# Optimization experiments

Hardware: AMD Instinct MI355X
Metric: run time of the kernel (lower is better)

Reference implementation:

```python
import jax, jax.numpy as jnp
import numpy as np

B, N, D, H, G = 4, 2048, 384, 8, 512
K = 8            # knn neighbors (hardcoded in get_graph_feature)
HID = 4 * D      # mlp_ratio = 4
FIN = 3 + G      # fuse_mlp in_features


def _ln(x, g, b, eps=1e-5):
    m = x.mean(-1, keepdims=True)
    v = ((x - m) ** 2).mean(-1, keepdims=True)
    return (x - m) * jax.lax.rsqrt(v + eps) * g + b


def _self_attn(x, qkv_w, pw, pb):
    b, n, c = x.shape
    hd = c // H
    qkv = (x @ qkv_w).reshape(b, n, 3, H, hd).transpose(2, 0, 3, 1, 4)
    q, k, v = qkv[0], qkv[1], qkv[2]                      # [b,h,n,hd]
    a = jax.nn.softmax(jnp.einsum('bhnd,bhmd->bhnm', q, k) * hd ** -0.5, -1)
    o = jnp.einsum('bhnm,bhmd->bhnd', a, v).transpose(0, 2, 1, 3).reshape(b, n, c)
    return o @ pw + pb


def _cross_attn(q, v, qw, kw, vw, pw, pb):
    b, n, c = q.shape
    nk = v.shape[1]
    hd = c // H
    qh = (q @ qw).reshape(b, n, H, hd).transpose(0, 2, 1, 3)
    kh = (v @ kw).reshape(b, nk, H, hd).transpose(0, 2, 1, 3)
    vh = (v @ vw).reshape(b, nk, H, hd).transpose(0, 2, 1, 3)
    a = jax.nn.softmax(jnp.einsum('bhnd,bhmd->bhnm', qh, kh) * hd ** -0.5, -1)
    o = jnp.einsum('bhnm,bhmd->bhnd', a, vh).transpose(0, 2, 1, 3).reshape(b, n, c)
    return o @ pw + pb


def _graph_feature(x, knn_index, x_q=None):
    b, n, c = x.shape
    nq = x_q.shape[1] if x_q is not None else n
    feat = x.reshape(b * n, c)[knn_index.reshape(-1)].reshape(b, K, nq, c)
    xq = (x_q if x_q is not None else x)[:, None, :, :]   # [b,1,nq,c]
    return jnp.concatenate([feat - xq, jnp.broadcast_to(xq, feat.shape)], -1)


def setup_inputs():
    key = jax.random.key(0)
    ks = iter(jax.random.split(key, 32))
    nrm = lambda shape: jax.random.normal(next(ks), shape, jnp.float32) * 0.02
    f32 = jnp.float32
    inp = {
        'q': jax.random.normal(next(ks), (B, D, N), f32),
        'in_pos': jax.random.normal(next(ks), (B, 3, N), f32),
        'guide_coding': jax.random.normal(next(ks), (B, G), f32),
        'norm1_g': jnp.ones((D,), f32), 'norm1_b': jnp.zeros((D,), f32),
        'qkv_w': nrm((D, 3 * D)),
        'sa_proj_w': nrm((D, D)), 'sa_proj_b': jnp.zeros((D,), f32),
        'normq_g': jnp.ones((D,), f32), 'normq_b': jnp.zeros((D,), f32),
        'fuse1_w': nrm((FIN, FIN)), 'fuse1_b': jnp.zeros((FIN,), f32),
        'fuse2_w': nrm((FIN, D)), 'fuse2_b': jnp.zeros((D,), f32),
        'normv_g': jnp.ones((D,), f32), 'normv_b': jnp.zeros((D,), f32),
        'ca_q_w': nrm((D, D)), 'ca_k_w': nrm((D, D)), 'ca_v_w': nrm((D, D)),
        'ca_proj_w': nrm((D, D)), 'ca_proj_b': jnp.zeros((D,), f32),
        'norm2_g': jnp.ones((D,), f32), 'norm2_b': jnp.zeros((D,), f32),
        'mlp1_w': nrm((D, HID)), 'mlp1_b': jnp.zeros((HID,), f32),
        'mlp2_w': nrm((HID, D)), 'mlp2_b': jnp.zeros((D,), f32),
        'knn_w': nrm((2 * D, D)), 'knn_b': jnp.zeros((D,), f32),
        'merge_w': nrm((2 * D, D)), 'merge_b': jnp.zeros((D,), f32),
        'knnx_w': nrm((2 * D, D)), 'knnx_b': jnp.zeros((D,), f32),
        'mergex_w': nrm((2 * D, D)), 'mergex_b': jnp.zeros((D,), f32),
        'self_knn_index': jax.random.randint(next(ks), (B, K, N), 0, B * N),
        'cross_knn_index': jax.random.randint(next(ks), (B, K, N), 0, B * N),
    }
    return inp


def reference(q, in_pos, guide_coding, norm1_g, norm1_b, qkv_w, sa_proj_w, sa_proj_b,
              normq_g, normq_b, fuse1_w, fuse1_b, fuse2_w, fuse2_b, normv_g, normv_b,
              ca_q_w, ca_k_w, ca_v_w, ca_proj_w, ca_proj_b, norm2_g, norm2_b,
              mlp1_w, mlp1_b, mlp2_w, mlp2_b, knn_w, knn_b, merge_w, merge_b,
              knnx_w, knnx_b, mergex_w, mergex_b, self_knn_index, cross_knn_index):
    npoints = in_pos.shape[2]
    q = q.transpose(0, 2, 1)                              # [B,N,D]
    norm_q = _ln(q, norm1_g, norm1_b)
    q_1 = _self_attn(norm_q, qkv_w, sa_proj_w, sa_proj_b)
    # build v from positions + broadcast guide coding
    gc = jnp.broadcast_to(guide_coding[:, :, None], (q.shape[0], G, npoints))
    v = jnp.concatenate([in_pos, gc], axis=1).transpose(0, 2, 1)  # [B,N,3+G]
    v = jax.nn.gelu(v @ fuse1_w + fuse1_b, approximate=False) @ fuse2_w + fuse2_b
    # self knn branch
    knn_f = _graph_feature(norm_q, self_knn_index)        # [B,K,N,2D]
    knn_f = jax.nn.leaky_relu(knn_f @ knn_w + knn_b, 0.2).max(axis=1)
    q_1 = jnp.concatenate([q_1, knn_f], -1) @ merge_w + merge_b
    q = q + q_1
    norm_q = _ln(q, normq_g, normq_b)
    norm_v = _ln(v, normv_g, normv_b)
    q_2 = _cross_attn(norm_q, norm_v, ca_q_w, ca_k_w, ca_v_w, ca_proj_w, ca_proj_b)
    # cross knn branch
    knn_f = _graph_feature(norm_v, cross_knn_index, norm_q)
    knn_f = jax.nn.leaky_relu(knn_f @ knnx_w + knnx_b, 0.2).max(axis=1)
    q_2 = jnp.concatenate([q_2, knn_f], -1) @ mergex_w + mergex_b
    q = q + q_2
    h = _ln(q, norm2_g, norm2_b)
    q = q + (jax.nn.gelu(h @ mlp1_w + mlp1_b, approximate=False) @ mlp2_w + mlp2_b)
    return q.transpose(0, 2, 1)                           # [B,D,N]
```

## Files before the change

### kernel.cpp

```cpp
#include <hip/hip_runtime.h>
#include <cstdint>
#include <cstddef>

#define B_ 4
#define N_ 2048
#define D_ 384
#define H_ 8
#define HD_ 48
#define G_ 512
#define K_ 8
#define HID_ 1536
#define FIN_ 515
#define FINP_ 576
#define M_ (B_*N_)
#define QSCALE 0.20823512f

typedef unsigned short u16;
typedef __attribute__((ext_vector_type(8))) short bf16x8;
typedef __attribute__((ext_vector_type(4))) float f32x4;

#define GLOAD16(gp, lp) __builtin_amdgcn_global_load_lds( \
    (const __attribute__((address_space(1))) void*)(gp), \
    (__attribute__((address_space(3))) void*)(lp), 16, 0, 0)

__device__ __forceinline__ u16 f2bf(float x){
  unsigned u = __builtin_bit_cast(unsigned, x);
  unsigned r = (u + 0x7fffu + ((u >> 16) & 1u)) >> 16;
  return (u16)r;
}
__device__ __forceinline__ float bf2f(u16 v){
  unsigned u = ((unsigned)v) << 16;
  return __builtin_bit_cast(float, u);
}
__device__ __forceinline__ float exp2_hw(float x){
  float r;
  asm("v_exp_f32 %0, %1" : "=v"(r) : "v"(x));
  return r;
}
__device__ __forceinline__ float gelu_f(float x){
  return 0.5f*x*(1.f + erff(x*0.70710678118654752f));
}

__global__ __launch_bounds__(256) void transpose_k(const float* __restrict__ in,
    float* __restrict__ out, int R, int C){
  __shared__ float tile[32][33];
  int b = blockIdx.z;
  int c0 = blockIdx.x<<5, r0 = blockIdx.y<<5;
  const float* ip = in + (size_t)b*R*C;
  float* op = out + (size_t)b*R*C;
  int tx = threadIdx.x, ty = threadIdx.y;
  #pragma unroll
  for (int i = ty; i < 32; i += 8)
    tile[i][tx] = ip[(size_t)(r0+i)*C + c0 + tx];
  __syncthreads();
  #pragma unroll
  for (int i = ty; i < 32; i += 8)
    op[(size_t)(c0+i)*R + r0 + tx] = tile[tx][i];
}

struct WJob { const float* src; u16* dst; int Kd, Nd, Kp, diff, Np, nbx, blk0; };
struct WJobs { WJob j[16]; };

__global__ __launch_bounds__(256) void wtconv_all(WJobs J){
  int b = blockIdx.x, ji = 0;
  #pragma unroll
  for (int i=1;i<16;i++) if (b >= J.j[i].blk0) ji = i;
  WJob jb = J.j[ji];
  int local = b - jb.blk0;
  int bx = local % jb.nbx, by = local / jb.nbx;
  __shared__ float tile[32][33];
  int k0 = bx<<5, n0 = by<<5;
  int tx = threadIdx.x, ty = threadIdx.y;
  #pragma unroll
  for (int i = ty; i < 32; i += 8){
    int k = k0+i, n = n0+tx;
    float v = 0.f;
    if (k < jb.Kd && n < jb.Nd){
      v = jb.src[(size_t)k*jb.Nd + n];
      if (jb.diff) v = jb.src[(size_t)(k+jb.diff)*jb.Nd + n] - v;
    }
    tile[i][tx] = v;
  }
  __syncthreads();
  #pragma unroll
  for (int i = ty; i < 32; i += 8){
    int n = n0+i, k = k0+tx;
    if (n < jb.Np && k < jb.Kp) jb.dst[(size_t)n*jb.Kp + k] = f2bf(tile[tx][i]);
  }
}

struct WP { const float *pw, *mwt, *pb, *mb2; u16* W; float* Bo; };
__global__ __launch_bounds__(256) void wprod_k(WP a, WP b){
  WP w = blockIdx.y ? b : a;
  int idx = blockIdx.x*256 + threadIdx.x;
  if (idx >= 385*384) return;
  int n = idx % 384, kk = idx / 384;
  float acc = 0.f;
  if (kk < 384){
    for (int j=0;j<384;j++) acc += w.pw[(size_t)kk*384+j] * w.mwt[(size_t)j*384+n];
    w.W[(size_t)n*768 + kk] = f2bf(acc);
  } else {
    for (int j=0;j<384;j++) acc += w.pb[j] * w.mwt[(size_t)j*384+n];
    w.Bo[n] = acc + w.mb2[n];
  }
}

__global__ __launch_bounds__(256) void biasfill_k(const float* __restrict__ knnb,
    const float* __restrict__ knnxb, float* __restrict__ bws){
  int i = blockIdx.x*256 + threadIdx.x;
  if (i < 2688){
    float v = 0.f;
    if (i >= 1536 && i < 1920) v = knnb[i-1536];
    else if (i >= 2304) v = knnxb[i-2304];
    bws[i] = v;
  }
}

__device__ __forceinline__ void ln_body(const float* xr, const float* g,
    const float* bta, u16* yr, float* sbuf, int t){
  float v0 = xr[t], v1 = xr[t+128], v2 = xr[t+256];
  float s = v0+v1+v2;
  #pragma unroll
  for (int off=32; off>0; off>>=1) s += __shfl_down(s, off, 64);
  int lane = t & 63, w = t >> 6;
  if (lane==0) sbuf[w] = s;
  __syncthreads();
  float mean = (sbuf[0]+sbuf[1]) * (1.f/(float)D_);
  float d0 = v0-mean, d1 = v1-mean, d2 = v2-mean;
  float s2 = d0*d0 + d1*d1 + d2*d2;
  #pragma unroll
  for (int off=32; off>0; off>>=1) s2 += __shfl_down(s2, off, 64);
  __syncthreads();
  if (lane==0) sbuf[w] = s2;
  __syncthreads();
  float inv = rsqrtf((sbuf[0]+sbuf[1])*(1.f/(float)D_) + 1e-5f);
  yr[t]     = f2bf(d0*inv*g[t]     + bta[t]);
  yr[t+128] = f2bf(d1*inv*g[t+128] + bta[t+128]);
  yr[t+256] = f2bf(d2*inv*g[t+256] + bta[t+256]);
}

__global__ __launch_bounds__(128) void ln_bf(const float* __restrict__ x,
    const float* __restrict__ g, const float* __restrict__ bta, u16* __restrict__ y){
  __shared__ float sbuf[2];
  int row = blockIdx.x;
  ln_body(x + (size_t)row*D_, g, bta, y + (size_t)row*D_, sbuf, threadIdx.x);
}

__global__ __launch_bounds__(128) void ln2_bf(const float* __restrict__ x0,
    const float* __restrict__ g0, const float* __restrict__ b0, u16* __restrict__ y0,
    const float* __restrict__ x1, const float* __restrict__ g1,
    const float* __restrict__ b1, u16* __restrict__ y1){
  __shared__ float sbuf[2];
  int row = blockIdx.x;
  if (row < M_)
    ln_body(x0 + (size_t)row*D_, g0, b0, y0 + (size_t)row*D_, sbuf, threadIdx.x);
  else {
    row -= M_;
    ln_body(x1 + (size_t)row*D_, g1, b1, y1 + (size_t)row*D_, sbuf, threadIdx.x);
  }
}

template<int ACT, int OUTBF, int ACCUM, int HASBIAS, int SCALEQ>
__global__ __launch_bounds__(512) void gemm8(const u16* __restrict__ A, int lda,
    const u16* __restrict__ Wt, int ldw, const float* __restrict__ bias,
    float* __restrict__ Cf, u16* __restrict__ Cb, int ldc, int Kd, int Nd, int Npad){
  __shared__ char Lmem[33280];
  u16* As = (u16*)Lmem;
  u16* Bs = As + 128*64;
  float* cred = (float*)Lmem;
  const int t = threadIdx.x;
  const int wv = t>>6, l = t&63;
  const int kg = wv>>2, wq = wv&3;
  const int wm = wq&1, wn = wq>>1;
  const int lr = l&15, ls = l>>4;
  const int bm = blockIdx.y<<7, bn = blockIdx.x<<6;
  f32x4 z4 = {0.f,0.f,0.f,0.f};
  f32x4 acc[4][2];
  #pragma unroll
  for (int mi=0;mi<4;mi++){ acc[mi][0]=z4; acc[mi][1]=z4; }
  int ago[2];
  #pragma unroll
  for (int i=0;i<2;i++){
    int g = t + (i<<9);
    int row = g>>3, slot = g&7;
    ago[i] = row*lda + ((slot ^ (row&7))<<3);
  }
  int bgo;
  {
    int row = t>>3, slot = t&7;
    bgo = row*ldw + ((slot ^ (row&7))<<3);
  }
  const u16* Abase = A + (size_t)bm*lda;
  const u16* Bbase = Wt + (size_t)bn*ldw;
  for (int k0=0; k0<Kd; k0+=64){
    #pragma unroll
    for (int i=0;i<2;i++)
      GLOAD16(Abase + k0 + ago[i], (char*)As + ((t + (i<<9))<<4));
    GLOAD16(Bbase + k0 + bgo, (char*)Bs + (t<<4));
    __syncthreads();
    bf16x8 af[4], bfr[2];
    #pragma unroll
    for (int mi=0;mi<4;mi++){
      int row = wm*64 + mi*16 + lr;
      int ss = (kg*4 + ls) ^ (row&7);
      af[mi] = *reinterpret_cast<bf16x8*>((char*)As + row*128 + ss*16);
    }
    #pragma unroll
    for (int ni=0;ni<2;ni++){
      int row = wn*32 + ni*16 + lr;
      int ss = (kg*4 + ls) ^ (row&7);
      bfr[ni] = *reinterpret_cast<bf16x8*>((char*)Bs + row*128 + ss*16);
    }
    #pragma unroll
    for (int mi=0;mi<4;mi++)
      #pragma unroll
      for (int ni=0;ni<2;ni++)
        acc[mi][ni] = __builtin_amdgcn_mfma_f32_16x16x32_bf16(af[mi], bfr[ni], acc[mi][ni], 0,0,0);
    __syncthreads();
  }
  if (kg == 1){
    #pragma unroll
    for (int mi=0;mi<4;mi++)
      #pragma unroll
      for (int ni=0;ni<2;ni++)
        #pragma unroll
        for (int r=0;r<4;r++){
          int row = wm*64 + mi*16 + ls*4 + r;
          int col = wn*32 + ni*16 + lr;
          cred[row*65 + col] = acc[mi][ni][r];
        }
  }
  __syncthreads();
  if (kg == 0){
    #pragma unroll
    for (int mi=0;mi<4;mi++){
      #pragma unroll
      for (int ni=0;ni<2;ni++){
        #pragma unroll
        for (int r=0;r<4;r++){
          int rl = wm*64 + mi*16 + ls*4 + r;
          int cl = wn*32 + ni*16 + lr;
          int row = bm + rl, col = bn + cl;
          float v = acc[mi][ni][r] + cred[rl*65 + cl];
          if (col < Nd){
            if (SCALEQ && col < 384) v *= QSCALE;
            if (HASBIAS) v += bias[col];
            if (ACT) v = gelu_f(v);
            if (OUTBF) Cb[(size_t)row*ldc + col] = f2bf(v);
            else if (ACCUM) Cf[(size_t)row*ldc + col] += v;
            else Cf[(size_t)row*ldc + col] = v;
          } else if (OUTBF && col < Npad){
            Cb[(size_t)row*ldc + col] = 0;
          }
        }
      }
    }
  }
}

__global__ __launch_bounds__(256) void vt_k(const u16* __restrict__ X, int ld,
                                            u16* __restrict__ Vt){
  __shared__ u16 tl[64][72];
  int bh = blockIdx.y, b = bh>>3, h = bh&7;
  int n0 = blockIdx.x<<6;
  #pragma unroll
  for (int i=0;i<2;i++){
    int g = threadIdx.x + (i<<8);
    if (g < 384){
      int r = g/6, c = (g - r*6)*8;
      *reinterpret_cast<float4*>(&tl[r][c]) =
        *reinterpret_cast<const float4*>(X + (size_t)(b*N_ + n0 + r)*ld + h*HD_ + c);
    }
  }
  __syncthreads();
  #pragma unroll
  for (int i=0;i<2;i++){
    int g = threadIdx.x + (i<<8);
    if (g < 384){
      int d = g % 48, sb = g / 48;
      int hf = (n0>>6)&1;
      int kt0 = n0 & ~127;
      size_t rowb = ((size_t)(bh*HD_+d))*N_ + kt0;
      int kA = hf*64 + sb*8;
      ushort4 va, vb;
      va.x = tl[sb*8+0][d]; va.y = tl[sb*8+1][d];
      va.z = tl[sb*8+2][d]; va.w = tl[sb*8+3][d];
      vb.x = tl[sb*8+4][d]; vb.y = tl[sb*8+5][d];
      vb.z = tl[sb*8+6][d]; vb.w = tl[sb*8+7][d];
      int uA = ((kA>>5)<<2) | ((kA>>2)&3);
      int pA = (((uA ^ (d&15)))<<3) + (((kA>>4)&1)<<2);
      int kB = kA + 4;
      int uB = ((kB>>5)<<2) | ((kB>>2)&3);
      int pB = (((uB ^ (d&15)))<<3) + (((kB>>4)&1)<<2);
      *reinterpret_cast<ushort4*>(Vt + rowb + pA) = va;
      *reinterpret_cast<ushort4*>(Vt + rowb + pB) = vb;
    }
  }
}

__global__ __launch_bounds__(256) void attn_mfma(const u16* __restrict__ Qp, int ldq,
    const u16* __restrict__ Kp, int ldk, const u16* __restrict__ Vt,
    u16* __restrict__ O, int ldo){
  __shared__ __align__(16) char KVls[2][28672];
  const int t = threadIdx.x, wv = t>>6, l = t&63;
  const int lr = l&15, ls = l>>4;
  const int bh = blockIdx.y, bb = bh>>3, h = bh&7;
  const int q0 = blockIdx.x<<6;
  bf16x8 zf = {0,0,0,0,0,0,0,0};
  f32x4 z4 = {0.f,0.f,0.f,0.f};
  const size_t rowQ = ((size_t)(bb*N_ + q0 + wv*16 + lr))*ldq + h*HD_;
  bf16x8 qa0 = *reinterpret_cast<const bf16x8*>(Qp + rowQ + 8*ls);
  bf16x8 qa1 = (ls < 2) ? *reinterpret_cast<const bf16x8*>(Qp + rowQ + 32 + 8*ls) : zf;
  f32x4 oacc[3] = {z4, z4, z4};
  float mrun = -1.0e30f, lrun = 0.f;

  const u16* Kbase = Kp + (size_t)(bb*N_)*ldk + h*HD_;
  const u16* Vbase = Vt + (size_t)bh*HD_*N_;
  int kgo[4];
  #pragma unroll
  for (int i=0;i<4;i++){
    int g = t + (i<<8);
    int key = g>>3, s = g&7;
    kgo[i] = key*ldk + ((s ^ (key&7))<<3);
  }
  int vgo[3];
  #pragma unroll
  for (int i=0;i<3;i++){
    int g = t + (i<<8);
    int d = g>>4, s = g&15;
    vgo[i] = d*N_ + (s<<3);
  }

  auto stage = [&](int kt, char* buf){
    const u16* kp = Kbase + (size_t)kt*128*ldk;
    #pragma unroll
    for (int i=0;i<4;i++)
      GLOAD16(kp + kgo[i], buf + ((t + (i<<8))<<4));
    const u16* vp = Vbase + kt*128;
    #pragma unroll
    for (int i=0;i<3;i++)
      GLOAD16(vp + vgo[i], buf + 16384 + ((t + (i<<8))<<4));
  };

  stage(0, KVls[0]);
  for (int kt = 0; kt < N_/128; kt++){
    char* cbuf = KVls[kt&1];
    if (kt+1 < N_/128){
      stage(kt+1, KVls[(kt+1)&1]);
      asm volatile("s_waitcnt vmcnt(7)" ::: "memory");
    } else {
      asm volatile("s_waitcnt vmcnt(0)" ::: "memory");
    }
    __builtin_amdgcn_sched_barrier(0);
    __builtin_amdgcn_s_barrier();
    __builtin_amdgcn_sched_barrier(0);
    f32x4 S[8];
    __builtin_amdgcn_s_setprio(1);
    #pragma unroll
    for (int sub=0; sub<8; sub++){
      int krow = sub*16 + lr;
      bf16x8 kb0 = *reinterpret_cast<bf16x8*>(cbuf + krow*128 + ((ls ^ (krow&7))<<4));
      bf16x8 kb1 = *reinterpret_cast<bf16x8*>(cbuf + krow*128 + (((4+ls) ^ (krow&7))<<4));
      f32x4 s = __builtin_amdgcn_mfma_f32_16x16x32_bf16(kb0, qa0, z4, 0,0,0);
      S[sub] = __builtin_amdgcn_mfma_f32_16x16x32_bf16(kb1, qa1, s, 0,0,0);
    }
    __builtin_amdgcn_s_setprio(0);
    float tm = fmaxf(fmaxf(fmaxf(S[0][0],S[0][1]), fmaxf(S[0][2],S[0][3])),
                     fmaxf(fmaxf(S[1][0],S[1][1]), fmaxf(S[1][2],S[1][3])));
    #pragma unroll
    for (int sub=2;sub<8;sub++)
      tm = fmaxf(tm, fmaxf(fmaxf(S[sub][0],S[sub][1]), fmaxf(S[sub][2],S[sub][3])));
    if (__all(tm - mrun <= 10.f)){
      float ps = 0.f;
      #pragma unroll
      for (int sub=0;sub<8;sub++)
        #pragma unroll
        for (int r=0;r<4;r++){
          float p = exp2_hw(S[sub][r]-mrun);
          S[sub][r] = p; ps += p;
        }
      lrun += ps;
    } else {
      float mx = fmaxf(tm, __shfl_xor(tm, 16, 64));
      mx = fmaxf(mx, __shfl_xor(mx, 32, 64));
      float mnew = fmaxf(mrun, mx);
      float al = exp2_hw(mrun - mnew);
      mrun = mnew;
      float ps = 0.f;
      #pragma unroll
      for (int sub=0;sub<8;sub++)
        #pragma unroll
        for (int r=0;r<4;r++){
          float p = exp2_hw(S[sub][r]-mnew);
          S[sub][r] = p; ps += p;
        }
      lrun = lrun*al + ps;
      #pragma unroll
      for (int r=0;r<4;r++){
        float alq = __shfl(al, ls*4 + r, 64);
        oacc[0][r] *= alq; oacc[1][r] *= alq; oacc[2][r] *= alq;
      }
    }
    union PU { unsigned u[4]; bf16x8 v; };
    PU pa[4];
    #pragma unroll
    for (int kb=0;kb<4;kb++){
      asm("v_cvt_pk_bf16_f32 %0, %1, %2" : "=v"(pa[kb].u[0]) : "v"(S[2*kb][0]),   "v"(S[2*kb][1]));
      asm("v_cvt_pk_bf16_f32 %0, %1, %2" : "=v"(pa[kb].u[1]) : "v"(S[2*kb][2]),   "v"(S[2*kb][3]));
      asm("v_cvt_pk_bf16_f32 %0, %1, %2" : "=v"(pa[kb].u[2]) : "v"(S[2*kb+1][0]), "v"(S[2*kb+1][1]));
      asm("v_cvt_pk_bf16_f32 %0, %1, %2" : "=v"(pa[kb].u[3]) : "v"(S[2*kb+1][2]), "v"(S[2*kb+1][3]));
    }
    __builtin_amdgcn_s_setprio(1);
    #pragma unroll
    for (int ni=0;ni<3;ni++){
      int d = ni*16 + lr;
      #pragma unroll
      for (int kb=0;kb<4;kb++){
        bf16x8 vb = *reinterpret_cast<bf16x8*>(cbuf + 16384 + d*256 + ((((kb*4+ls) ^ (d&15)))<<4));
        oacc[ni] = __builtin_amdgcn_mfma_f32_16x16x32_bf16(pa[kb].v, vb, oacc[ni], 0,0,0);
      }
    }
    __builtin_amdgcn_s_setprio(0);
    __builtin_amdgcn_sched_barrier(0);
    __builtin_amdgcn_s_barrier();
    __builtin_amdgcn_sched_barrier(0);
  }
  float sden = lrun;
  sden += __shfl_xor(sden, 16, 64);
  sden += __shfl_xor(sden, 32, 64);
  #pragma unroll
  for (int r=0;r<4;r++){
    float dq = __shfl(sden, ls*4 + r, 64);
    float inv = 1.f / dq;
    size_t orow = (size_t)(bb*N_ + q0 + wv*16 + ls*4 + r);
    #pragma unroll
    for (int ni=0;ni<3;ni++)
      O[orow*ldo + h*HD_ + ni*16 + lr] = f2bf(oacc[ni][r] * inv);
  }
}

__global__ __launch_bounds__(384) void gather_max_bf(const u16* __restrict__ P, int ldp,
    const u16* __restrict__ Q2, int ldq2, const int* __restrict__ idx,
    u16* __restrict__ out, int ldo){
  int m = blockIdx.x;
  int d = threadIdx.x;
  int b = m >> 11, n = m & (N_-1);
  float q2 = bf2f(Q2[(size_t)m*ldq2 + d]);
  float mx = -3.0e38f;
  #pragma unroll
  for (int k=0;k<K_;k++){
    int j = idx[((b<<3) + k)*N_ + n];
    float val = bf2f(P[(size_t)j*ldp + d]) + q2;
    val = (val >= 0.f) ? val : 0.2f*val;
    mx = fmaxf(mx, val);
  }
  out[(size_t)m*ldo + d] = f2bf(mx);
}

__global__ __launch_bounds__(256) void build_v(const float* __restrict__ pos,
    const float* __restrict__ gc, u16* __restrict__ v){
  int m = blockIdx.x;
  int b = m >> 11, n = m & (N_-1);
  for (int c = threadIdx.x; c < FINP_; c += 256){
    float val = 0.f;
    if (c < 3) val = pos[(b*3 + c)*N_ + n];
    else if (c < FIN_) val = gc[(b<<9) + (c-3)];
    v[(size_t)m*FINP_ + c] = f2bf(val);
  }
}

extern "C" void kernel_launch(void* const* d_in, const int* in_sizes, int n_in,
                              void* d_out, int out_size, void* d_ws, size_t ws_size,
                              hipStream_t stream){
  const float* q_in   = (const float*)d_in[0];
  const float* in_pos = (const float*)d_in[1];
  const float* guide  = (const float*)d_in[2];
  const float* n1g = (const float*)d_in[3];
  const float* n1b = (const float*)d_in[4];
  const float* qkv_w = (const float*)d_in[5];
  const float* sa_pw = (const float*)d_in[6];
  const float* sa_pb = (const float*)d_in[7];
  const float* nqg = (const float*)d_in[8];
  const float* nqb = (const float*)d_in[9];
  const float* f1w = (const float*)d_in[10];
  const float* f1b = (const float*)d_in[11];
  const float* f2w = (const float*)d_in[12];
  const float* f2b = (const float*)d_in[13];
  const float* nvg = (const float*)d_in[14];
  const float* nvb = (const float*)d_in[15];
  const float* caqw = (const float*)d_in[16];
  const float* cakw = (const float*)d_in[17];
  const float* cavw = (const float*)d_in[18];
  const float* capw = (const float*)d_in[19];
  const float* capb = (const float*)d_in[20];
  const float* n2g = (const float*)d_in[21];
  const float* n2b = (const float*)d_in[22];
  const float* m1w = (const float*)d_in[23];
  const float* m1b = (const float*)d_in[24];
  const float* m2w = (const float*)d_in[25];
  const float* m2b = (const float*)d_in[26];
  const float* knnw = (const float*)d_in[27];
  const float* knnb = (const float*)d_in[28];
  const float* mw = (const float*)d_in[29];
  const float* mb = (const float*)d_in[30];
  const float* knnxw = (const float*)d_in[31];
  const float* knnxb = (const float*)d_in[32];
  const float* mxw = (const float*)d_in[33];
  const float* mxb = (const float*)d_in[34];
  const int* sidx = (const int*)d_in[35];
  const int* cidx = (const int*)d_in[36];
  float* out = (float*)d_out;

  const size_t MD = (size_t)M_*D_;
  float* q_cur = (float*)d_ws;
  float* vbuf  = q_cur + MD;
  u16* R     = (u16*)(vbuf + MD);
  u16* nq_bf = R + (size_t)M_*1920;
  u16* nv_bf = nq_bf + MD;
  u16* cc    = nv_bf + MD;
  u16* vin   = cc + (size_t)M_*768;
  u16* e2    = vin + (size_t)M_*FINP_;
  u16* Vt    = e2 + (size_t)M_*FINP_;
  u16* wb    = Vt + (size_t)32*HD_*N_;
  u16* W1    = wb;  wb += (size_t)1920*384;
  u16* Wq    = wb;  wb += (size_t)768*384;
  u16* Wv    = wb;  wb += (size_t)1152*384;
  u16* Wfold = wb;  wb += (size_t)384*768;
  u16* Wfoldx= wb;  wb += (size_t)384*768;
  u16* f1T   = wb;  wb += (size_t)FINP_*FINP_;
  u16* f2T   = wb;  wb += (size_t)384*FINP_;
  u16* m1T   = wb;  wb += (size_t)1536*384;
  u16* m2T   = wb;  wb += (size_t)384*1536;
  if (((uintptr_t)wb & 3) != 0) wb++;
  float* bias_ws = (float*)wb;
  const size_t needed = (char*)(bias_ws + 3456) - (char*)d_ws;
  if (ws_size < needed) return;

  u16* X1 = R;
  u16* Xq = R;
  u16* Xv = R + (size_t)M_*768;
  u16* hid = R;

  dim3 tb32(32,8);
  transpose_k<<<dim3(N_/32, D_/32, B_), tb32, 0, stream>>>(q_in, q_cur, D_, N_);
  WJobs J;
  auto setj = [&](int i, const float* src, u16* dst, int Kd, int Nd, int Kp, int diff, int Np){
    J.j[i].src = src; J.j[i].dst = dst; J.j[i].Kd = Kd; J.j[i].Nd = Nd;
    J.j[i].Kp = Kp; J.j[i].diff = diff; J.j[i].Np = Np;
    J.j[i].nbx = (Kp+31)/32; J.j[i].blk0 = 0;
  };
  setj(0,  qkv_w, W1,                    384, 1152, 384, 0,   1152);
  setj(1,  knnw,  W1 + (size_t)1152*384, 384, 384, 384, 0,    384);
  setj(2,  knnw,  W1 + (size_t)1536*384, 384, 384, 384, 384,  384);
  setj(3,  caqw,  Wq,                    384, 384, 384, 0,    384);
  setj(4,  knnxw, Wq + (size_t)384*384,  384, 384, 384, 384,  384);
  setj(5,  cakw,  Wv,                    384, 384, 384, 0,    384);
  setj(6,  cavw,  Wv + (size_t)384*384,  384, 384, 384, 0,    384);
  setj(7,  knnxw, Wv + (size_t)768*384,  384, 384, 384, 0,    384);
  setj(8,  mw  + (size_t)384*384, Wfold  + 384, 384, 384, 768, 0, 384);
  setj(9,  mxw + (size_t)384*384, Wfoldx + 384, 384, 384, 768, 0, 384);
  setj(10, f1w,   f1T, FIN_, FIN_, FINP_, 0, FINP_);
  setj(11, f2w,   f2T, FIN_, 384, FINP_, 0,  384);
  setj(12, m1w,   m1T, 384, 1536, 384, 0,    1536);
  setj(13, m2w,   m2T, 1536, 384, 1536, 0,   384);
  int tot = 0;
  for (int i=0;i<14;i++){ J.j[i].blk0 = tot; tot += J.j[i].nbx * ((J.j[i].Np+31)/32); }
  J.j[14] = J.j[13]; J.j[14].blk0 = 0x7fffffff; J.j[14].nbx = 1;
  J.j[15] = J.j[14];
  wtconv_all<<<tot, tb32, 0, stream>>>(J);
  WP wpa = { sa_pw, mw,  sa_pb, mb,  Wfold,  bias_ws + 2688 };
  WP wpb = { capw,  mxw, capb,  mxb, Wfoldx, bias_ws + 3072 };
  wprod_k<<<dim3(578, 2), 256, 0, stream>>>(wpa, wpb);
  biasfill_k<<<11, 256, 0, stream>>>(knnb, knnxb, bias_ws);
  ln_bf<<<M_, 128, 0, stream>>>(q_cur, n1g, n1b, nq_bf);
  gemm8<0,1,0,1,1><<<dim3(30, 64), 512, 0, stream>>>(nq_bf, 384, W1, 384, bias_ws, nullptr, X1, 1920, 384, 1920, 1920);
  vt_k<<<dim3(32, 32), 256, 0, stream>>>(X1 + 768, 1920, Vt);
  attn_mfma<<<dim3(32, 32), 256, 0, stream>>>(X1, 1920, X1 + 384, 1920, Vt, cc, 768);
  gather_max_bf<<<M_, 384, 0, stream>>>(X1 + 1152, 1920, X1 + 1536, 1920, sidx, cc + 384, 768);
  gemm8<0,0,1,1,0><<<dim3(6, 64), 512, 0, stream>>>(cc, 768, Wfold, 768, bias_ws + 2688, q_cur, nullptr, 384, 768, 384, 384);
  build_v<<<M_, 256, 0, stream>>>(in_pos, guide, vin);
  gemm8<1,1,0,1,0><<<dim3(9, 64), 512, 0, stream>>>(vin, FINP_, f1T, FINP_, f1b, nullptr, e2, FINP_, FINP_, FIN_, FINP_);
  gemm8<0,0,0,1,0><<<dim3(6, 64), 512, 0, stream>>>(e2, FINP_, f2T, FINP_, f2b, vbuf, nullptr, 384, FINP_, 384, 384);
  ln2_bf<<<2*M_, 128, 0, stream>>>(q_cur, nqg, nqb, nq_bf, vbuf, nvg, nvb, nv_bf);
  gemm8<0,1,0,1,1><<<dim3(12, 64), 512, 0, stream>>>(nq_bf, 384, Wq, 384, bias_ws + 1920, nullptr, Xq, 768, 384, 768, 768);
  gemm8<0,1,0,0,0><<<dim3(18, 64), 512, 0, stream>>>(nv_bf, 384, Wv, 384, nullptr, nullptr, Xv, 1152, 384, 1152, 1152);
  vt_k<<<dim3(32, 32), 256, 0, stream>>>(Xv + 384, 1152, Vt);
  attn_mfma<<<dim3(32, 32), 256, 0, stream>>>(Xq, 768, Xv, 1152, Vt, cc, 768);
  gather_max_bf<<<M_, 384, 0, stream>>>(Xv + 768, 1152, Xq + 384, 768, cidx, cc + 384, 768);
  gemm8<0,0,1,1,0><<<dim3(6, 64), 512, 0, stream>>>(cc, 768, Wfoldx, 768, bias_ws + 3072, q_cur, nullptr, 384, 768, 384, 384);
  ln_bf<<<M_, 128, 0, stream>>>(q_cur, n2g, n2b, nq_bf);
  gemm8<1,1,0,1,0><<<dim3(24, 64), 512, 0, stream>>>(nq_bf, 384, m1T, 384, m1b, nullptr, hid, 1536, 384, 1536, 1536);
  gemm8<0,0,1,1,0><<<dim3(6, 64), 512, 0, stream>>>(hid, 1536, m2T, 1536, m2b, q_cur, nullptr, 384, 1536, 384, 384);
  transpose_k<<<dim3(D_/32, N_/32, B_), tb32, 0, stream>>>(q_cur, out, N_, D_);
}
```

Baseline: 459.5 us.

## Double-buffer gemm8 LDS tiles to overlap global loads with MFMA

Splits the gemm8 shared-memory tile into two 24 KB buffers and issues the next K-slice's global-to-LDS loads before computing on the current slice. Each step waits with a partial vmcnt so loads stay in flight, and the barriers are raw s_barrier calls fenced by sched_barrier. The MFMA block is also wrapped in s_setprio to favour compute waves. LDS use rises from about 33 KB to 48 KB per block, which can lower occupancy, and the hand-written wait counts must match the number of loads issued per stage.

```diff
diff --git a/kernel.cpp b/kernel.cpp
--- a/kernel.cpp
+++ b/kernel.cpp
@@ -164,9 +164,7 @@
 __global__ __launch_bounds__(512) void gemm8(const u16* __restrict__ A, int lda,
     const u16* __restrict__ Wt, int ldw, const float* __restrict__ bias,
     float* __restrict__ Cf, u16* __restrict__ Cb, int ldc, int Kd, int Nd, int Npad){
-  __shared__ char Lmem[33280];
-  u16* As = (u16*)Lmem;
-  u16* Bs = As + 128*64;
+  __shared__ __align__(16) char Lmem[49152];
   float* cred = (float*)Lmem;
   const int t = threadIdx.x;
   const int wv = t>>6, l = t&63;
@@ -192,31 +190,48 @@
   }
   const u16* Abase = A + (size_t)bm*lda;
   const u16* Bbase = Wt + (size_t)bn*ldw;
-  for (int k0=0; k0<Kd; k0+=64){
+  auto stage = [&](int k0, char* buf){
     #pragma unroll
     for (int i=0;i<2;i++)
-      GLOAD16(Abase + k0 + ago[i], (char*)As + ((t + (i<<9))<<4));
-    GLOAD16(Bbase + k0 + bgo, (char*)Bs + (t<<4));
-    __syncthreads();
+      GLOAD16(Abase + k0 + ago[i], buf + ((t + (i<<9))<<4));
+    GLOAD16(Bbase + k0 + bgo, buf + 16384 + (t<<4));
+  };
+  stage(0, Lmem);
+  int it = 0;
+  for (int k0=0; k0<Kd; k0+=64, it^=1){
+    char* cbuf = Lmem + it*24576;
+    if (k0+64 < Kd){
+      stage(k0+64, Lmem + (it^1)*24576);
+      asm volatile("s_waitcnt vmcnt(3)" ::: "memory");
+    } else {
+      asm volatile("s_waitcnt vmcnt(0)" ::: "memory");
+    }
+    __builtin_amdgcn_sched_barrier(0);
+    __builtin_amdgcn_s_barrier();
+    __builtin_amdgcn_sched_barrier(0);
     bf16x8 af[4], bfr[2];
     #pragma unroll
     for (int mi=0;mi<4;mi++){
       int row = wm*64 + mi*16 + lr;
       int ss = (kg*4 + ls) ^ (row&7);
-      af[mi] = *reinterpret_cast<bf16x8*>((char*)As + row*128 + ss*16);
+      af[mi] = *reinterpret_cast<bf16x8*>(cbuf + row*128 + ss*16);
     }
     #pragma unroll
     for (int ni=0;ni<2;ni++){
       int row = wn*32 + ni*16 + lr;
       int ss = (kg*4 + ls) ^ (row&7);
-      bfr[ni] = *reinterpret_cast<bf16x8*>((char*)Bs + row*128 + ss*16);
-    }
+      bfr[ni] = *reinterpret_cast<bf16x8*>(cbuf + 16384 + row*128 + ss*16);
+    }
+    __builtin_amdgcn_s_setprio(1);
     #pragma unroll
     for (int mi=0;mi<4;mi++)
       #pragma unroll
       for (int ni=0;ni<2;ni++)
         acc[mi][ni] = __builtin_amdgcn_mfma_f32_16x16x32_bf16(af[mi], bfr[ni], acc[mi][ni], 0,0,0);
-    __syncthreads();
+    __builtin_amdgcn_s_setprio(0);
+    __builtin_amdgcn_sched_barrier(0);
+    __builtin_amdgcn_s_barrier();
+    __builtin_amdgcn_sched_barrier(0);
   }
   if (kg == 1){
     #pragma unroll
```

Measured after the change: 463.3 us. About the same (+0.8%).

## Add 128x128 four-wave GEMM kernel for wide bf16-output projections

Applied to the files above, without the earlier changes.

Adds a new GEMM kernel with 128x128 output tiles computed by four waves, each owning a 64x64 sub-tile. Operands go straight into XOR-swizzled LDS via direct global-to-LDS loads, with no split-K reduction through shared memory. It replaces the older 64-column, 512-thread kernel for the wide bf16-output projections (qkv/knn, cross q, cross kv, fuse1, mlp1) to get more data reuse per tile and fewer blocks. The fuse1 weight is padded to 640 columns so its N dimension divides by 128. The kernel has no double buffering, so load latency is exposed between K steps.

```diff
diff --git a/kernel.cpp b/kernel.cpp
--- a/kernel.cpp
+++ b/kernel.cpp
@@ -252,6 +252,88 @@
           } else if (OUTBF && col < Npad){
             Cb[(size_t)row*ldc + col] = 0;
           }
+        }
+      }
+    }
+  }
+}
+
+template<int ACT, int OUTBF, int HASBIAS, int SCALEQ>
+__global__ __launch_bounds__(256) void gemm4w(const u16* __restrict__ A, int lda,
+    const u16* __restrict__ Wt, int ldw, const float* __restrict__ bias,
+    u16* __restrict__ Cb, int ldc, int Kd, int Nd, int Npad){
+  __shared__ __align__(16) char Lmem[32768];
+  const int t = threadIdx.x;
+  const int wv = t>>6, l = t&63;
+  const int wr = wv&1, wc = wv>>1;
+  const int lr = l&15, ls = l>>4;
+  const int bm = blockIdx.y<<7, bn = blockIdx.x<<7;
+  f32x4 z4 = {0.f,0.f,0.f,0.f};
+  f32x4 acc[4][4];
+  #pragma unroll
+  for (int mi=0;mi<4;mi++)
+    #pragma unroll
+    for (int ni=0;ni<4;ni++) acc[mi][ni] = z4;
+  int ago[4], bgo[4];
+  #pragma unroll
+  for (int i=0;i<4;i++){
+    int g = t + (i<<8);
+    int row = g>>3, slot = g&7;
+    int so = (slot ^ (row&7))<<3;
+    ago[i] = row*lda + so;
+    bgo[i] = row*ldw + so;
+  }
+  const u16* Abase = A + (size_t)bm*lda;
+  const u16* Bbase = Wt + (size_t)bn*ldw;
+  for (int k0=0; k0<Kd; k0+=64){
+    #pragma unroll
+    for (int i=0;i<4;i++)
+      GLOAD16(Abase + k0 + ago[i], Lmem + ((t + (i<<8))<<4));
+    #pragma unroll
+    for (int i=0;i<4;i++)
+      GLOAD16(Bbase + k0 + bgo[i], Lmem + 16384 + ((t + (i<<8))<<4));
+    __syncthreads();
+    #pragma unroll
+    for (int ks=0; ks<2; ks++){
+      bf16x8 af[4], bfr[4];
+      #pragma unroll
+      for (int mi=0;mi<4;mi++){
+        int row = wr*64 + mi*16 + lr;
+        int ss = (ks*4 + ls) ^ (row&7);
+        af[mi] = *reinterpret_cast<bf16x8*>(Lmem + row*128 + ss*16);
+      }
+      #pragma unroll
+      for (int ni=0;ni<4;ni++){
+        int row = wc*64 + ni*16 + lr;
+        int ss = (ks*4 + ls) ^ (row&7);
+        bfr[ni] = *reinterpret_cast<bf16x8*>(Lmem + 16384 + row*128 + ss*16);
+      }
+      __builtin_amdgcn_s_setprio(1);
+      #pragma unroll
+      for (int mi=0;mi<4;mi++)
+        #pragma unroll
+        for (int ni=0;ni<4;ni++)
+          acc[mi][ni] = __builtin_amdgcn_mfma_f32_16x16x32_bf16(af[mi], bfr[ni], acc[mi][ni], 0,0,0);
+      __builtin_amdgcn_s_setprio(0);
+    }
+    __syncthreads();
+  }
+  #pragma unroll
+  for (int mi=0;mi<4;mi++){
+    #pragma unroll
+    for (int ni=0;ni<4;ni++){
+      #pragma unroll
+      for (int r=0;r<4;r++){
+        int row = bm + wr*64 + mi*16 + ls*4 + r;
+        int col = bn + wc*64 + ni*16 + lr;
+        float v = acc[mi][ni][r];
+        if (col < Nd){
+          if (SCALEQ && col < 384) v *= QSCALE;
+          if (HASBIAS) v += bias[col];
+          if (ACT) v = gelu_f(v);
+          Cb[(size_t)row*ldc + col] = f2bf(v);
+        } else if (col < Npad){
+          Cb[(size_t)row*ldc + col] = 0;
         }
       }
     }
@@ -527,7 +609,7 @@
   u16* Wv    = wb;  wb += (size_t)1152*384;
   u16* Wfold = wb;  wb += (size_t)384*768;
   u16* Wfoldx= wb;  wb += (size_t)384*768;
-  u16* f1T   = wb;  wb += (size_t)FINP_*FINP_;
+  u16* f1T   = wb;  wb += (size_t)640*FINP_;
   u16* f2T   = wb;  wb += (size_t)384*FINP_;
   u16* m1T   = wb;  wb += (size_t)1536*384;
   u16* m2T   = wb;  wb += (size_t)384*1536;
@@ -559,7 +641,7 @@
   setj(7,  knnxw, Wv + (size_t)768*384,  384, 384, 384, 0,    384);
   setj(8,  mw  + (size_t)384*384, Wfold  + 384, 384, 384, 768, 0, 384);
   setj(9,  mxw + (size_t)384*384, Wfoldx + 384, 384, 384, 768, 0, 384);
-  setj(10, f1w,   f1T, FIN_, FIN_, FINP_, 0, FINP_);
+  setj(10, f1w,   f1T, FIN_, FIN_, FINP_, 0, 640);
   setj(11, f2w,   f2T, FIN_, 384, FINP_, 0,  384);
   setj(12, m1w,   m1T, 384, 1536, 384, 0,    1536);
   setj(13, m2w,   m2T, 1536, 384, 1536, 0,   384);
@@ -573,23 +655,23 @@
   wprod_k<<<dim3(578, 2), 256, 0, stream>>>(wpa, wpb);
   biasfill_k<<<11, 256, 0, stream>>>(knnb, knnxb, bias_ws);
   ln_bf<<<M_, 128, 0, stream>>>(q_cur, n1g, n1b, nq_bf);
-  gemm8<0,1,0,1,1><<<dim3(30, 64), 512, 0, stream>>>(nq_bf, 384, W1, 384, bias_ws, nullptr, X1, 1920, 384, 1920, 1920);
+  gemm4w<0,1,1,1><<<dim3(15, 64), 256, 0, stream>>>(nq_bf, 384, W1, 384, bias_ws, X1, 1920, 384, 1920, 1920);
   vt_k<<<dim3(32, 32), 256, 0, stream>>>(X1 + 768, 1920, Vt);
   attn_mfma<<<dim3(32, 32), 256, 0, stream>>>(X1, 1920, X1 + 384, 1920, Vt, cc, 768);
   gather_max_bf<<<M_, 384, 0, stream>>>(X1 + 1152, 1920, X1 + 1536, 1920, sidx, cc + 384, 768);
   gemm8<0,0,1,1,0><<<dim3(6, 64), 512, 0, stream>>>(cc, 768, Wfold, 768, bias_ws + 2688, q_cur, nullptr, 384, 768, 384, 384);
   build_v<<<M_, 256, 0, stream>>>(in_pos, guide, vin);
-  gemm8<1,1,0,1,0><<<dim3(9, 64), 512, 0, stream>>>(vin, FINP_, f1T, FINP_, f1b, nullptr, e2, FINP_, FINP_, FIN_, FINP_);
+  gemm4w<1,1,1,0><<<dim3(5, 64), 256, 0, stream>>>(vin, FINP_, f1T, FINP_, f1b, e2, FINP_, FINP_, FIN_, FINP_);
   gemm8<0,0,0,1,0><<<dim3(6, 64), 512, 0, stream>>>(e2, FINP_, f2T, FINP_, f2b, vbuf, nullptr, 384, FINP_, 384, 384);
   ln2_bf<<<2*M_, 128, 0, stream>>>(q_cur, nqg, nqb, nq_bf, vbuf, nvg, nvb, nv_bf);
-  gemm8<0,1,0,1,1><<<dim3(12, 64), 512, 0, stream>>>(nq_bf, 384, Wq, 384, bias_ws + 1920, nullptr, Xq, 768, 384, 768, 768);
-  gemm8<0,1,0,0,0><<<dim3(18, 64), 512, 0, stream>>>(nv_bf, 384, Wv, 384, nullptr, nullptr, Xv, 1152, 384, 1152, 1152);
+  gemm4w<0,1,1,1><<<dim3(6, 64), 256, 0, stream>>>(nq_bf, 384, Wq, 384, bias_ws + 1920, Xq, 768, 384, 768, 768);
+  gemm4w<0,1,0,0><<<dim3(9, 64), 256, 0, stream>>>(nv_bf, 384, Wv, 384, nullptr, Xv, 1152, 384, 1152, 1152);
   vt_k<<<dim3(32, 32), 256, 0, stream>>>(Xv + 384, 1152, Vt);
   attn_mfma<<<dim3(32, 32), 256, 0, stream>>>(Xq, 768, Xv, 1152, Vt, cc, 768);
   gather_max_bf<<<M_, 384, 0, stream>>>(Xv + 768, 1152, Xq + 384, 768, cidx, cc + 384, 768);
   gemm8<0,0,1,1,0><<<dim3(6, 64), 512, 0, stream>>>(cc, 768, Wfoldx, 768, bias_ws + 3072, q_cur, nullptr, 384, 768, 384, 384);
   ln_bf<<<M_, 128, 0, stream>>>(q_cur, n2g, n2b, nq_bf);
-  gemm8<1,1,0,1,0><<<dim3(24, 64), 512, 0, stream>>>(nq_bf, 384, m1T, 384, m1b, nullptr, hid, 1536, 384, 1536, 1536);
+  gemm4w<1,1,1,0><<<dim3(12, 64), 256, 0, stream>>>(nq_bf, 384, m1T, 384, m1b, hid, 1536, 384, 1536, 1536);
   gemm8<0,0,1,1,0><<<dim3(6, 64), 512, 0, stream>>>(hid, 1536, m2T, 1536, m2b, q_cur, nullptr, 384, 1536, 384, 384);
   transpose_k<<<dim3(D_/32, N_/32, B_), tb32, 0, stream>>>(q_cur, out, N_, D_);
 }
```

Measured after the change: 525.6 us. 14.4% more time.
